# Optimization experiments

Hardware: AMD Instinct MI355X
Metric: run time of the kernel (lower is better)

Reference implementation:

```python
import jax, jax.numpy as jnp
import numpy as np

V = 1.0e10           # large init value for non-seed pixels (FastGeodis v)
LAMB = 0.0           # lamb=0 => pure Euclidean raster-scan distance
ITERS = 2            # FastGeodis iterations
THRESH = 0.7         # binarize_map threshold
TOPO_WEIGHT = 0.005
TOPO_WINDOW = 64
EPS = 1e-6
BIG = 1e20


def _sweep_down(dist, image):
    # One top-down raster sweep of the FastGeodis up-down pass.
    # dist, image: [H, W]. Row r updates from row r-1 at col offsets {-1,0,+1}
    # with squared spatial distances {2,1,2}; lamb weights the intensity term.
    W = dist.shape[1]
    sp2 = (2.0, 1.0, 2.0)

    def step(carry, xs):
        pd, pi = carry          # previous-row distance / intensity, [W]
        d_row, i_row = xs
        pd_pad = jnp.pad(pd, 1, constant_values=BIG)
        pi_pad = jnp.pad(pi, 1, constant_values=0.0)
        new = d_row
        for k in range(3):
            p = pd_pad[k:k + W]
            q = i_row - pi_pad[k:k + W]
            new = jnp.minimum(new, p + jnp.sqrt(sp2[k] + LAMB * q * q))
        return (new, i_row), new

    (_, _), rest = jax.lax.scan(step, (dist[0], image[0]), (dist[1:], image[1:]))
    return jnp.concatenate([dist[:1], rest], axis=0)


def _updown(dist, image):
    dist = _sweep_down(dist, image)
    dist = _sweep_down(dist[::-1], image[::-1])[::-1]
    return dist


def generalised_geodesic2d(image, softmask):
    # image: intensity map [H,W]; softmask: [H,W]; dist init = V * softmask.
    dist = V * softmask
    for _ in range(ITERS):
        dist = _updown(dist, image)
        dist = _updown(dist.T, image.T).T
    return dist


def calculate_edt(inp):
    # Original: softmask = inp, intensity image = 1 - inp (mask_pt = 1 - image_pt).
    return generalised_geodesic2d(1.0 - inp, inp)


def _global_norm(x):
    return (x - x.min()) / (x.max() - x.min() + EPS)


def _topo_loss(p, t, window):
    # Persistence-style matching proxy: within each non-overlapping window,
    # match level-set values of pred and target by sorting (0-dim persistence
    # birth/death values of the filtration are order statistics of the window)
    # and penalize squared differences of matched values.
    H, W = p.shape
    nh, nw = H // window, W // window

    def win_sort(x):
        x = x.reshape(nh, window, nw, window).transpose(0, 2, 1, 3)
        return jnp.sort(x.reshape(nh * nw, window * window), axis=-1)

    return jnp.mean((win_sort(p) - win_sort(t)) ** 2)


def _per_item(pred_i, target_i):
    # pred_i/target_i: [C, H, W]; pred already remapped to [0, 1]
    bin_pred = (pred_i >= THRESH).astype(jnp.float32)
    comb_pred = jnp.max(bin_pred, axis=0)        # combine_channels
    comb_tgt = jnp.max(target_i, axis=0)
    edt_p = _global_norm(calculate_edt(1.0 - comb_pred))
    edt_t = _global_norm(calculate_edt(1.0 - comb_tgt))
    return _topo_loss(edt_p, edt_t, TOPO_WINDOW)


def setup_inputs():
    key = jax.random.key(0)
    k1, k2 = jax.random.split(key)
    B, C, H, W = 16, 3, 512, 512
    pred = jax.random.normal(k1, (B, C, H, W), dtype=jnp.float32)  # model output in ~[-1,1]
    # target: binary multi-channel cell masks (sparse foreground)
    target = (jax.random.uniform(k2, (B, C, H, W)) > 0.8).astype(jnp.float32)
    return {"pred": pred, "target": target}


def reference(pred, target):
    pred01 = (pred + 1.0) / 2.0
    losses = jax.vmap(_per_item)(pred01.astype(jnp.float32), target.astype(jnp.float32))
    mean_loss = losses.mean()
    return (mean_loss * TOPO_WEIGHT, mean_loss)
```

## Files before the change

### kernel.cpp

```cpp
#include <hip/hip_runtime.h>

#define BIGF 1e20f
#define VF   1e10f

constexpr float SQ2 = 1.41421356237309515f;

__device__ __forceinline__ float dpp_left(float x)
{
    int o = __builtin_amdgcn_update_dpp(0x60AD78ECu , __float_as_int(x),
                                        0x138, 0xF, 0xF, false);
    return __int_as_float(o);
}
__device__ __forceinline__ float dpp_right(float x)
{
    int o = __builtin_amdgcn_update_dpp(0x60AD78ECu , __float_as_int(x),
                                        0x130, 0xF, 0xF, false);
    return __int_as_float(o);
}
template<int CTRL>
__device__ __forceinline__ float qdpp(float x)
{
    return __int_as_float(__builtin_amdgcn_update_dpp(0, __float_as_int(x),
                                                      CTRL, 0xF, 0xF, true));
}
__device__ __forceinline__ float fmed3(float a, float b, float c)
{
    return __builtin_amdgcn_fmed3f(a, b, c);
}

__device__ __forceinline__ void load_row8(const float* __restrict__ M, int r, int c0, float v[8])
{
    const float4* q = (const float4*)(M + ((long)r << 9) + c0);
    float4 a = q[0], b = q[1];
    v[0] = a.x; v[1] = a.y; v[2] = a.z; v[3] = a.w;
    v[4] = b.x; v[5] = b.y; v[6] = b.z; v[7] = b.w;
}

__device__ __forceinline__ void step8(const float cur[8], const float p[8], float nv[8])
{
    float left  = dpp_left(p[7]);
    float right = dpp_right(p[0]);
    #pragma unroll
    for (int j = 0; j < 8; ++j) {
        float l  = (j == 0) ? left  : p[j - 1];
        float rr = (j == 7) ? right : p[j + 1];
        nv[j] = fminf(fminf(cur[j], p[j] + 1.0f), fminf(l, rr) + SQ2);
    }
}

__global__ __launch_bounds__(256) void k_init(const float* __restrict__ pred,
                                              const float* __restrict__ tgt,
                                              float* __restrict__ bufA,
                                              float* __restrict__ acc,
                                              unsigned* __restrict__ count,
                                              float* __restrict__ minmax)
{
    if (blockIdx.x == 0 && threadIdx.x == 0) { *acc = 0.0f; *count = 0u; }
    if (blockIdx.x == 0 && threadIdx.x < 64)
        minmax[threadIdx.x] = (threadIdx.x & 1) ? 0.0f : BIGF;

    int r = blockIdx.x & 7;
    int k = blockIdx.x >> 3;
    int b = r + 8 * (k >> 8);
    int pix = ((k & 255) * 256 + threadIdx.x) << 2;
    long base = (long)b * 3 * 262144 + pix;

    float4 p0 = *(const float4*)(pred + base);
    float4 p1 = *(const float4*)(pred + base + 262144);
    float4 p2 = *(const float4*)(pred + base + 2 * 262144);
    float4 t0 = *(const float4*)(tgt + base);
    float4 t1 = *(const float4*)(tgt + base + 262144);
    float4 t2 = *(const float4*)(tgt + base + 2 * 262144);

    float P0[4] = {p0.x, p0.y, p0.z, p0.w};
    float P1[4] = {p1.x, p1.y, p1.z, p1.w};
    float P2[4] = {p2.x, p2.y, p2.z, p2.w};
    float T0[4] = {t0.x, t0.y, t0.z, t0.w};
    float T1[4] = {t1.x, t1.y, t1.z, t1.w};
    float T2[4] = {t2.x, t2.y, t2.z, t2.w};

    float oP[4], oT[4];
    #pragma unroll
    for (int e = 0; e < 4; ++e) {
        bool fgP = ((P0[e] + 1.0f) * 0.5f >= 0.7f) ||
                   ((P1[e] + 1.0f) * 0.5f >= 0.7f) ||
                   ((P2[e] + 1.0f) * 0.5f >= 0.7f);
        float mt = fmaxf(fmaxf(T0[e], T1[e]), T2[e]);
        oP[e] = fgP ? 0.0f : VF;
        oT[e] = VF * (1.0f - mt);
    }
    *(float4*)(bufA + (long)b * 262144 + pix)        = make_float4(oP[0], oP[1], oP[2], oP[3]);
    *(float4*)(bufA + (long)(16 + b) * 262144 + pix) = make_float4(oT[0], oT[1], oT[2], oT[3]);
}

__global__ __launch_bounds__(64) void k_p1d(const float* __restrict__ X0,
                                            float* __restrict__ Cb)
{
    int bi = blockIdx.x, m = bi >> 4, w = bi & 15;
    const float* X = X0 + ((long)m << 18);
    int c0 = (int)threadIdx.x << 3, a = w << 5;
    float p[8]; load_row8(X, a, c0, p);
    float buf[8][8];
    #pragma unroll
    for (int k = 1; k <= 7; ++k) load_row8(X, a + k, c0, buf[k & 7]);
    #pragma unroll
    for (int i = 1; i < 32; ++i) {
        if (i + 7 < 32) load_row8(X, a + i + 7, c0, buf[(i + 7) & 7]);
        float nv[8]; step8(buf[i & 7], p, nv);
        #pragma unroll
        for (int j = 0; j < 8; ++j) p[j] = nv[j];
    }
    float4* o = (float4*)(Cb + m * 8192 + w * 512 + c0);
    o[0] = make_float4(p[0], p[1], p[2], p[3]);
    o[1] = make_float4(p[4], p[5], p[6], p[7]);
}

__device__ __forceinline__ void combine(float* __restrict__ bwp, float* __restrict__ part,
                                        int wdst, int wsrc, int t, int wave, int lane,
                                        const float wreg[8])
{
    const float* bs = bwp + wsrc * 576;
    if (wave <= 8) {
        int base = lane * 8 + 8 * wave;
        float W[16];
        float4 W0 = *(const float4*)(bs + base);
        float4 W1 = *(const float4*)(bs + base + 4);
        W[0]=W0.x; W[1]=W0.y; W[2]=W0.z; W[3]=W0.w;
        W[4]=W1.x; W[5]=W1.y; W[6]=W1.z; W[7]=W1.w;
        float acc[8];
        if (wave < 8) {
            float4 W2 = *(const float4*)(bs + base + 8);
            float4 W3 = *(const float4*)(bs + base + 12);
            W[8]=W2.x; W[9]=W2.y; W[10]=W2.z; W[11]=W2.w;
            W[12]=W3.x; W[13]=W3.y; W[14]=W3.z; W[15]=W3.w;
            #pragma unroll
            for (int j = 0; j < 8; ++j) acc[j] = W[j] + wreg[0];
            #pragma unroll
            for (int dt = 1; dt < 8; ++dt)
                #pragma unroll
                for (int j = 0; j < 8; ++j)
                    acc[j] = fminf(acc[j], W[j + dt] + wreg[dt]);
        } else {
            #pragma unroll
            for (int j = 0; j < 8; ++j) acc[j] = W[j] + wreg[0];
        }
        float4* pp = (float4*)(part + wave * 512 + lane * 8);
        pp[0] = make_float4(acc[0], acc[1], acc[2], acc[3]);
        pp[1] = make_float4(acc[4], acc[5], acc[6], acc[7]);
    }
    __syncthreads();
    if (t < 512) {
        float r = bwp[wdst * 576 + 32 + t];
        #pragma unroll
        for (int p2 = 0; p2 < 9; ++p2) r = fminf(r, part[p2 * 512 + t]);
        bwp[wdst * 576 + 32 + t] = r;
    }
    __syncthreads();
}

__global__ __launch_bounds__(1024) void k_comb(float* __restrict__ Cb, int dir)
{
    __shared__ __align__(16) float bwp[16 * 576];
    __shared__ __align__(16) float part[9 * 512];
    __shared__ float wgt[72];
    int m = blockIdx.x, t = threadIdx.x, wave = t >> 6, lane = t & 63, c0 = lane << 3;
    float* Cm = Cb + m * 8192;

    bwp[wave * 576 + ((lane < 32) ? lane : lane + 512)] = BIGF;
    *(float4*)(bwp + wave * 576 + 32 + c0)     = *(const float4*)(Cm + wave * 512 + c0);
    *(float4*)(bwp + wave * 576 + 32 + c0 + 4) = *(const float4*)(Cm + wave * 512 + c0 + 4);
    if (t < 65) { int d = t - 32; int ad = d < 0 ? -d : d; wgt[t] = ad * SQ2 + (float)(32 - ad); }
    __syncthreads();
    float wreg[8];
    #pragma unroll
    for (int dt = 0; dt < 8; ++dt) wreg[dt] = BIGF;
    if (wave < 8) {
        #pragma unroll
        for (int dt = 0; dt < 8; ++dt) wreg[dt] = wgt[wave * 8 + dt];
    } else if (wave == 8) wreg[0] = wgt[64];

    #pragma unroll 1
    for (int i = 0; i < 15; ++i) {
        int w2 = (dir > 0) ? (1 + i) : (14 - i);
        combine(bwp, part, w2, w2 - dir, t, wave, lane, wreg);
    }
    *(float4*)(Cm + wave * 512 + c0)     = *(const float4*)(bwp + wave * 576 + 32 + c0);
    *(float4*)(Cm + wave * 512 + c0 + 4) = *(const float4*)(bwp + wave * 576 + 32 + c0 + 4);
}

__global__ __launch_bounds__(64) void k_pb(const float* __restrict__ X0,
                                           const float* __restrict__ Cb,
                                           float* __restrict__ Db)
{
    __shared__ __align__(16) float stash[31 * 512];
    int bi = blockIdx.x, m = bi >> 4, w = bi & 15;
    const float* X = X0 + ((long)m << 18);
    const int L = threadIdx.x;
    int c0 = L << 3, a = w << 5;
    float p[8], buf[8][8];

    if (w) {
        const float4* s = (const float4*)(Cb + m * 8192 + (w - 1) * 512 + c0);
        float4 s0 = s[0], s1 = s[1];
        p[0]=s0.x; p[1]=s0.y; p[2]=s0.z; p[3]=s0.w;
        p[4]=s1.x; p[5]=s1.y; p[6]=s1.z; p[7]=s1.w;
    } else {
        #pragma unroll
        for (int j = 0; j < 8; ++j) p[j] = BIGF;
    }

    #pragma unroll
    for (int k = 0; k < 7; ++k) load_row8(X, a + k, c0, buf[k & 7]);
    #pragma unroll
    for (int i = 0; i < 32; ++i) {
        if (i + 7 < 32) load_row8(X, a + i + 7, c0, buf[(i + 7) & 7]);
        float nv[8]; step8(buf[i & 7], p, nv);
        if (i < 31) {
            *(float4*)(stash + i * 512 + L * 4)       = make_float4(nv[0], nv[1], nv[2], nv[3]);
            *(float4*)(stash + i * 512 + 256 + L * 4) = make_float4(nv[4], nv[5], nv[6], nv[7]);
        }
        #pragma unroll
        for (int j = 0; j < 8; ++j) p[j] = nv[j];
    }

    float q[8], cur[8];
    #pragma unroll
    for (int j = 0; j < 8; ++j) q[j] = p[j];
    {
        float4 x0 = *(const float4*)(stash + 30 * 512 + L * 4);
        float4 x1 = *(const float4*)(stash + 30 * 512 + 256 + L * 4);
        cur[0]=x0.x; cur[1]=x0.y; cur[2]=x0.z; cur[3]=x0.w;
        cur[4]=x1.x; cur[5]=x1.y; cur[6]=x1.z; cur[7]=x1.w;
    }
    #pragma unroll
    for (int i = 1; i < 32; ++i) {
        float nxt[8];
        if (i < 31) {
            float4 x0 = *(const float4*)(stash + (30 - i) * 512 + L * 4);
            float4 x1 = *(const float4*)(stash + (30 - i) * 512 + 256 + L * 4);
            nxt[0]=x0.x; nxt[1]=x0.y; nxt[2]=x0.z; nxt[3]=x0.w;
            nxt[4]=x1.x; nxt[5]=x1.y; nxt[6]=x1.z; nxt[7]=x1.w;
        }
        float nv[8]; step8(cur, q, nv);
        #pragma unroll
        for (int j = 0; j < 8; ++j) q[j] = nv[j];
        if (i < 31) {
            #pragma unroll
            for (int j = 0; j < 8; ++j) cur[j] = nxt[j];
        }
    }
    float4* o = (float4*)(Db + m * 8192 + w * 512 + c0);
    o[0] = make_float4(q[0], q[1], q[2], q[3]);
    o[1] = make_float4(q[4], q[5], q[6], q[7]);
}

__device__ __forceinline__ void sst516(float* st, int slot, int c0, const float v[8])
{
    float4* q = (float4*)(st + slot * 516 + c0);
    q[0] = make_float4(v[0], v[1], v[2], v[3]);
    q[1] = make_float4(v[4], v[5], v[6], v[7]);
}
__device__ __forceinline__ void sld516(const float* st, int slot, int c0, float v[8])
{
    const float4* q = (const float4*)(st + slot * 516 + c0);
    float4 a = q[0], b = q[1];
    v[0]=a.x; v[1]=a.y; v[2]=a.z; v[3]=a.w;
    v[4]=b.x; v[5]=b.y; v[6]=b.z; v[7]=b.w;
}
__device__ __forceinline__ void half_out32(const float* st, float* __restrict__ Xo,
                                           int slotbase, int a2, int L)
{
    int g = L >> 2, j = (L & 3) << 2;
    #pragma unroll
    for (int it = 0; it < 32; ++it) {
        int c = (it << 4) + g;
        float4 v = make_float4(st[(slotbase + j + 0) * 516 + c],
                               st[(slotbase + j + 1) * 516 + c],
                               st[(slotbase + j + 2) * 516 + c],
                               st[(slotbase + j + 3) * 516 + c]);
        *(float4*)(Xo + (long)c * 512 + a2 + j) = v;
    }
}

__global__ __launch_bounds__(64) void k_p3u(const float* __restrict__ X0,
                                            float* __restrict__ Xo0,
                                            const float* __restrict__ Cb,
                                            const float* __restrict__ Db,
                                            float* __restrict__ minmax,
                                            int final_pass)
{
    __shared__ __align__(16) float stash[32 * 516];
    int bi = blockIdx.x, m = bi >> 4, w = bi & 15;
    const float* X = X0 + ((long)m << 18);
    float* Xo = Xo0 + ((long)m << 18);
    const int L = threadIdx.x;
    int c0 = L << 3, a = w << 5;
    float p[8], buf[8][8];

    if (w) {
        const float4* s = (const float4*)(Cb + m * 8192 + (w - 1) * 512 + c0);
        float4 s0 = s[0], s1 = s[1];
        p[0]=s0.x; p[1]=s0.y; p[2]=s0.z; p[3]=s0.w;
        p[4]=s1.x; p[5]=s1.y; p[6]=s1.z; p[7]=s1.w;
    } else {
        #pragma unroll
        for (int j = 0; j < 8; ++j) p[j] = BIGF;
    }
    #pragma unroll
    for (int k = 0; k < 7; ++k) load_row8(X, a + k, c0, buf[k & 7]);
    #pragma unroll
    for (int i = 0; i < 32; ++i) {
        if (i + 7 < 32) load_row8(X, a + i + 7, c0, buf[(i + 7) & 7]);
        float nv[8]; step8(buf[i & 7], p, nv);
        sst516(stash, i, c0, nv);
        #pragma unroll
        for (int j = 0; j < 8; ++j) p[j] = nv[j];
    }

    float s2[8];
    if (w < 15) {
        const float4* s = (const float4*)(Db + m * 8192 + (w + 1) * 512 + c0);
        float4 s0 = s[0], s1 = s[1];
        s2[0]=s0.x; s2[1]=s0.y; s2[2]=s0.z; s2[3]=s0.w;
        s2[4]=s1.x; s2[5]=s1.y; s2[6]=s1.z; s2[7]=s1.w;
    } else {
        #pragma unroll
        for (int j = 0; j < 8; ++j) s2[j] = BIGF;
    }
    float mn = BIGF, mx = -BIGF;
    #pragma unroll
    for (int i = 0; i < 16; ++i) {
        float cu[8];
        if (i == 0) {
            #pragma unroll
            for (int j = 0; j < 8; ++j) cu[j] = p[j];
        } else {
            sld516(stash, 31 - i, c0, cu);
        }
        float nv[8]; step8(cu, s2, nv);
        sst516(stash, 31 - i, c0, nv);
        #pragma unroll
        for (int j = 0; j < 8; ++j) { s2[j] = nv[j]; mn = fminf(mn, nv[j]); mx = fmaxf(mx, nv[j]); }
    }
    half_out32(stash, Xo, 16, a + 16, L);
    #pragma unroll
    for (int i = 16; i < 32; ++i) {
        float cu[8]; sld516(stash, 31 - i, c0, cu);
        float nv[8]; step8(cu, s2, nv);
        sst516(stash, 31 - i, c0, nv);
        #pragma unroll
        for (int j = 0; j < 8; ++j) { s2[j] = nv[j]; mn = fminf(mn, nv[j]); mx = fmaxf(mx, nv[j]); }
    }
    half_out32(stash, Xo, 0, a, L);

    if (final_pass) {
        for (int o = 32; o > 0; o >>= 1) {
            mn = fminf(mn, __shfl_down(mn, o));
            mx = fmaxf(mx, __shfl_down(mx, o));
        }
        if (L == 0) {
            atomicMin((int*)(minmax + 2 * m),     __float_as_int(mn));
            atomicMax((int*)(minmax + 2 * m + 1), __float_as_int(mx));
        }
    }
}

__device__ __forceinline__ void cex(float& lo, float& hi)
{
    float l = fminf(lo, hi);
    hi = fmaxf(lo, hi);
    lo = l;
}
__device__ __forceinline__ void merge8asc(float v[8])
{
    cex(v[0],v[4]); cex(v[1],v[5]); cex(v[2],v[6]); cex(v[3],v[7]);
    cex(v[0],v[2]); cex(v[1],v[3]); cex(v[4],v[6]); cex(v[5],v[7]);
    cex(v[0],v[1]); cex(v[2],v[3]); cex(v[4],v[5]); cex(v[6],v[7]);
}
__device__ __forceinline__ void sort8asc(float v[8])
{
    cex(v[0],v[1]); cex(v[2],v[3]); cex(v[4],v[5]); cex(v[6],v[7]);
    cex(v[0],v[3]); cex(v[1],v[2]); cex(v[4],v[7]); cex(v[5],v[6]);
    cex(v[0],v[1]); cex(v[2],v[3]); cex(v[4],v[5]); cex(v[6],v[7]);
    cex(v[0],v[7]); cex(v[1],v[6]); cex(v[2],v[5]); cex(v[3],v[4]);
    cex(v[0],v[2]); cex(v[1],v[3]); cex(v[4],v[6]); cex(v[5],v[7]);
    cex(v[0],v[1]); cex(v[2],v[3]); cex(v[4],v[5]); cex(v[6],v[7]);
}
__device__ __forceinline__ void xshfl(float v[8], int j8, float sel)
{
    #pragma unroll
    for (int e = 0; e < 8; ++e) {
        float o = __shfl_xor(v[e], j8);
        v[e] = fmed3(v[e], o, sel);
    }
}
template<int CTRL>
__device__ __forceinline__ void xdpp(float v[8], float sel)
{
    #pragma unroll
    for (int e = 0; e < 8; ++e) {
        float o = qdpp<CTRL>(v[e]);
        v[e] = fmed3(v[e], o, sel);
    }
}
__device__ __forceinline__ void rshfl(float v[8], int tmask, float sel)
{
    float o[8];
    #pragma unroll
    for (int e = 0; e < 8; ++e) o[e] = __shfl_xor(v[7 - e], tmask);
    #pragma unroll
    for (int e = 0; e < 8; ++e) v[e] = fmed3(v[e], o[e], sel);
}
template<int CTRL>
__device__ __forceinline__ void rdpp(float v[8], float sel)
{
    float o[8];
    #pragma unroll
    for (int e = 0; e < 8; ++e) o[e] = qdpp<CTRL>(v[7 - e]);
    #pragma unroll
    for (int e = 0; e < 8; ++e) v[e] = fmed3(v[e], o[e], sel);
}
__device__ __forceinline__ void lstage(float p[8], float q[8], int tmask, float sel, bool rev,
                                       float* sp, float* st, int t)
{
    __syncthreads();
    int sw = (t >> 2) & 1;
    int o0 = t * 8 + sw * 4;
    int o1 = t * 8 + (sw ^ 1) * 4;
    *(float4*)(sp + o0) = make_float4(p[0], p[1], p[2], p[3]);
    *(float4*)(sp + o1) = make_float4(p[4], p[5], p[6], p[7]);
    *(float4*)(st + o0) = make_float4(q[0], q[1], q[2], q[3]);
    *(float4*)(st + o1) = make_float4(q[4], q[5], q[6], q[7]);
    __syncthreads();
    int pt = t ^ tmask;
    int psw = (pt >> 2) & 1;
    int q0 = pt * 8 + psw * 4;
    int q1 = pt * 8 + (psw ^ 1) * 4;
    float4 a = *(const float4*)(sp + q0), bb = *(const float4*)(sp + q1);
    float4 c = *(const float4*)(st + q0), d = *(const float4*)(st + q1);
    float op[8] = {a.x,a.y,a.z,a.w,bb.x,bb.y,bb.z,bb.w};
    float oq[8] = {c.x,c.y,c.z,c.w,d.x,d.y,d.z,d.w};
    if (rev) {
        #pragma unroll
        for (int e = 0; e < 8; ++e) {
            p[e] = fmed3(p[e], op[7 - e], sel);
            q[e] = fmed3(q[e], oq[7 - e], sel);
        }
    } else {
        #pragma unroll
        for (int e = 0; e < 8; ++e) {
            p[e] = fmed3(p[e], op[e], sel);
            q[e] = fmed3(q[e], oq[e], sel);
        }
    }
}

__global__ __launch_bounds__(512) void k_loss(const float* __restrict__ bufB,
                                              const float* __restrict__ minmax,
                                              float* __restrict__ acc,
                                              unsigned* __restrict__ count,
                                              float* __restrict__ out)
{
    __shared__ float sp[4096];
    __shared__ float st[4096];
    __shared__ float rs[8];

    int t = threadIdx.x;
    int r = blockIdx.x & 7;
    int k = blockIdx.x >> 3;
    int b = r + 8 * (k >> 6);
    int w = k & 63;
    int wi = w >> 3, wj = w & 7;

    int i0 = t << 3;
    int y = wi * 64 + (i0 >> 6);
    int x = wj * 64 + (i0 & 63);

    float mnP = minmax[2 * b],        mxP = minmax[2 * b + 1];
    float mnT = minmax[2 * (16 + b)], mxT = minmax[2 * (16 + b) + 1];
    float sclP = 1.0f / (mxP - mnP + 1e-6f);
    float sclT = 1.0f / (mxT - mnT + 1e-6f);

    float p[8], q[8];
    {
        const float4* P4 = (const float4*)(bufB + (long)b * 262144 + y * 512 + x);
        const float4* T4 = (const float4*)(bufB + (long)(16 + b) * 262144 + y * 512 + x);
        float4 a = P4[0], bb = P4[1], c = T4[0], d = T4[1];
        p[0]=a.x; p[1]=a.y; p[2]=a.z; p[3]=a.w; p[4]=bb.x; p[5]=bb.y; p[6]=bb.z; p[7]=bb.w;
        q[0]=c.x; q[1]=c.y; q[2]=c.z; q[3]=c.w; q[4]=d.x;  q[5]=d.y;  q[6]=d.z;  q[7]=d.w;
        #pragma unroll
        for (int e = 0; e < 8; ++e) {
            p[e] = (p[e] - mnP) * sclP;
            q[e] = (q[e] - mnT) * sclT;
        }
    }

    const float INFP = __builtin_inff();
    sort8asc(p); sort8asc(q);

    #pragma unroll 1
    for (int kk = 16; kk <= 4096; kk <<= 1) {
        int tmask = (kk - 1) >> 3;
        float sel = ((t & (kk >> 4)) == 0) ? -INFP : INFP;
        if (kk == 16)        { rdpp<0xB1>(p, sel); rdpp<0xB1>(q, sel); }
        else if (kk == 32)   { rdpp<0x1B>(p, sel); rdpp<0x1B>(q, sel); }
        else if (tmask < 64) { rshfl(p, tmask, sel); rshfl(q, tmask, sel); }
        else                 lstage(p, q, tmask, sel, true, sp, st, t);

        #pragma unroll 1
        for (int j = kk >> 2; j >= 8; j >>= 1) {
            int j8 = j >> 3;
            float s2 = ((t & j8) == 0) ? -INFP : INFP;
            if (j8 == 1)      { xdpp<0xB1>(p, s2); xdpp<0xB1>(q, s2); }
            else if (j8 == 2) { xdpp<0x4E>(p, s2); xdpp<0x4E>(q, s2); }
            else if (j8 < 64) { xshfl(p, j8, s2); xshfl(q, j8, s2); }
            else              lstage(p, q, j8, s2, false, sp, st, t);
        }
        merge8asc(p); merge8asc(q);
    }

    float s = 0.0f;
    #pragma unroll
    for (int e = 0; e < 8; ++e) { float d = p[e] - q[e]; s += d * d; }
    for (int o = 32; o > 0; o >>= 1) s += __shfl_down(s, o);
    if ((t & 63) == 0) rs[t >> 6] = s;
    __syncthreads();
    if (t == 0) {
        float tot = 0.0f;
        #pragma unroll
        for (int i = 0; i < 8; ++i) tot += rs[i];
        atomicAdd(acc, tot);
        __threadfence();
        unsigned done = atomicAdd(count, 1u);
        if (done == 1023u) {
            float total = atomicAdd(acc, 0.0f);
            float mean = total * (1.0f / 4194304.0f);
            out[0] = mean * 0.005f;
            out[1] = mean;
        }
    }
}

extern "C" void kernel_launch(void* const* d_in, const int* in_sizes, int n_in,
                              void* d_out, int out_size, void* d_ws, size_t ws_size,
                              hipStream_t stream)
{
    const float* pred = (const float*)d_in[0];
    const float* tgt  = (const float*)d_in[1];
    float* out = (float*)d_out;

    char* ws = (char*)d_ws;
    float* bufA     = (float*)ws;
    float* bufB     = (float*)(ws + (32ull << 20));
    float* Cb       = (float*)(ws + (64ull << 20));
    float* Db       = (float*)(ws + (65ull << 20));
    float* minmax   = (float*)(ws + (66ull << 20));
    float* acc      = minmax + 64;
    unsigned* count = (unsigned*)(acc + 1);

    k_init<<<4096, 256, 0, stream>>>(pred, tgt, bufA, acc, count, minmax);

    for (int s = 0; s < 4; ++s) {
        const float* in = (s & 1) ? bufB : bufA;
        float* outb     = (s & 1) ? bufA : bufB;
        k_p1d <<<512,   64, 0, stream>>>(in, Cb);
        k_comb<<< 32, 1024, 0, stream>>>(Cb, +1);
        k_pb  <<<512,   64, 0, stream>>>(in, Cb, Db);
        k_comb<<< 32, 1024, 0, stream>>>(Db, -1);
        k_p3u <<<512,   64, 0, stream>>>(in, outb, Cb, Db, minmax, s == 3 ? 1 : 0);
    }

    k_loss<<<1024, 512, 0, stream>>>(bufA, minmax, acc, count, out);
}
```

Baseline: 385.7 us.

## Merge forward and backward block passes, derive backward carry-in algebraically in combine

The separate first-pass and backward-pass kernels are fused into one kernel. It computes each block's forward output from a BIG seed and also the backward result using local-only inputs. The second combine pass then corrects the backward values by min-plus propagation of the combined forward carries through a 64-wide distance kernel. This removes one full read of the image per stage and cuts the per-stage kernel launches from five to three. In exchange the combine kernel does more shared-memory work, and correctness relies on min-plus linearity of the sweep with the odd/even weight formula.

```diff
diff --git a/kernel.cpp b/kernel.cpp
--- a/kernel.cpp
+++ b/kernel.cpp
@@ -93,33 +93,75 @@
     *(float4*)(bufA + (long)(16 + b) * 262144 + pix) = make_float4(oT[0], oT[1], oT[2], oT[3]);
 }
 
-__global__ __launch_bounds__(64) void k_p1d(const float* __restrict__ X0,
-                                            float* __restrict__ Cb)
-{
+__global__ __launch_bounds__(64) void k_p1du(const float* __restrict__ X0,
+                                             float* __restrict__ Cb,
+                                             float* __restrict__ Db)
+{
+    __shared__ __align__(16) float stash[31 * 512];
     int bi = blockIdx.x, m = bi >> 4, w = bi & 15;
     const float* X = X0 + ((long)m << 18);
-    int c0 = (int)threadIdx.x << 3, a = w << 5;
-    float p[8]; load_row8(X, a, c0, p);
-    float buf[8][8];
-    #pragma unroll
-    for (int k = 1; k <= 7; ++k) load_row8(X, a + k, c0, buf[k & 7]);
-    #pragma unroll
-    for (int i = 1; i < 32; ++i) {
+    const int L = threadIdx.x;
+    int c0 = L << 3, a = w << 5;
+    float p[8], buf[8][8];
+    #pragma unroll
+    for (int j = 0; j < 8; ++j) p[j] = BIGF;
+
+    #pragma unroll
+    for (int k = 0; k < 7; ++k) load_row8(X, a + k, c0, buf[k & 7]);
+    #pragma unroll
+    for (int i = 0; i < 32; ++i) {
         if (i + 7 < 32) load_row8(X, a + i + 7, c0, buf[(i + 7) & 7]);
         float nv[8]; step8(buf[i & 7], p, nv);
+        if (i < 31) {
+            *(float4*)(stash + i * 512 + L * 4)       = make_float4(nv[0], nv[1], nv[2], nv[3]);
+            *(float4*)(stash + i * 512 + 256 + L * 4) = make_float4(nv[4], nv[5], nv[6], nv[7]);
+        }
         #pragma unroll
         for (int j = 0; j < 8; ++j) p[j] = nv[j];
     }
-    float4* o = (float4*)(Cb + m * 8192 + w * 512 + c0);
-    o[0] = make_float4(p[0], p[1], p[2], p[3]);
-    o[1] = make_float4(p[4], p[5], p[6], p[7]);
-}
-
+    {
+        float4* o = (float4*)(Cb + m * 8192 + w * 512 + c0);
+        o[0] = make_float4(p[0], p[1], p[2], p[3]);
+        o[1] = make_float4(p[4], p[5], p[6], p[7]);
+    }
+
+    float q[8], cur[8];
+    #pragma unroll
+    for (int j = 0; j < 8; ++j) q[j] = p[j];
+    {
+        float4 x0 = *(const float4*)(stash + 30 * 512 + L * 4);
+        float4 x1 = *(const float4*)(stash + 30 * 512 + 256 + L * 4);
+        cur[0]=x0.x; cur[1]=x0.y; cur[2]=x0.z; cur[3]=x0.w;
+        cur[4]=x1.x; cur[5]=x1.y; cur[6]=x1.z; cur[7]=x1.w;
+    }
+    #pragma unroll
+    for (int i = 1; i < 32; ++i) {
+        float nxt[8];
+        if (i < 31) {
+            float4 x0 = *(const float4*)(stash + (30 - i) * 512 + L * 4);
+            float4 x1 = *(const float4*)(stash + (30 - i) * 512 + 256 + L * 4);
+            nxt[0]=x0.x; nxt[1]=x0.y; nxt[2]=x0.z; nxt[3]=x0.w;
+            nxt[4]=x1.x; nxt[5]=x1.y; nxt[6]=x1.z; nxt[7]=x1.w;
+        }
+        float nv[8]; step8(cur, q, nv);
+        #pragma unroll
+        for (int j = 0; j < 8; ++j) q[j] = nv[j];
+        if (i < 31) {
+            #pragma unroll
+            for (int j = 0; j < 8; ++j) cur[j] = nxt[j];
+        }
+    }
+    float4* o = (float4*)(Db + m * 8192 + w * 512 + c0);
+    o[0] = make_float4(q[0], q[1], q[2], q[3]);
+    o[1] = make_float4(q[4], q[5], q[6], q[7]);
+}
+
+template<int S, int G>
 __device__ __forceinline__ void combine(float* __restrict__ bwp, float* __restrict__ part,
                                         int wdst, int wsrc, int t, int wave, int lane,
                                         const float wreg[8])
 {
-    const float* bs = bwp + wsrc * 576;
+    const float* bs = bwp + wsrc * S + (G - 32);
     if (wave <= 8) {
         int base = lane * 8 + 8 * wave;
         float W[16];
@@ -150,25 +192,32 @@
     }
     __syncthreads();
     if (t < 512) {
-        float r = bwp[wdst * 576 + 32 + t];
+        float r = bwp[wdst * S + G + t];
         #pragma unroll
         for (int p2 = 0; p2 < 9; ++p2) r = fminf(r, part[p2 * 512 + t]);
-        bwp[wdst * 576 + 32 + t] = r;
-    }
-    __syncthreads();
-}
-
-__global__ __launch_bounds__(1024) void k_comb(float* __restrict__ Cb, int dir)
-{
-    __shared__ __align__(16) float bwp[16 * 576];
+        bwp[wdst * S + G + t] = r;
+    }
+    __syncthreads();
+}
+
+__global__ __launch_bounds__(1024) void k_comb2(float* __restrict__ Cb,
+                                                float* __restrict__ Db)
+{
+    __shared__ __align__(16) float bwpA[16 * 640];
+    __shared__ __align__(16) float bwpB[16 * 576];
     __shared__ __align__(16) float part[9 * 512];
     __shared__ float wgt[72];
     int m = blockIdx.x, t = threadIdx.x, wave = t >> 6, lane = t & 63, c0 = lane << 3;
     float* Cm = Cb + m * 8192;
-
-    bwp[wave * 576 + ((lane < 32) ? lane : lane + 512)] = BIGF;
-    *(float4*)(bwp + wave * 576 + 32 + c0)     = *(const float4*)(Cm + wave * 512 + c0);
-    *(float4*)(bwp + wave * 576 + 32 + c0 + 4) = *(const float4*)(Cm + wave * 512 + c0 + 4);
+    float* Dm = Db + m * 8192;
+
+    bwpA[wave * 640 + lane]       = BIGF;
+    bwpA[wave * 640 + 576 + lane] = BIGF;
+    bwpB[wave * 576 + ((lane < 32) ? lane : lane + 512)] = BIGF;
+    *(float4*)(bwpA + wave * 640 + 64 + c0)     = *(const float4*)(Cm + wave * 512 + c0);
+    *(float4*)(bwpA + wave * 640 + 64 + c0 + 4) = *(const float4*)(Cm + wave * 512 + c0 + 4);
+    *(float4*)(bwpB + wave * 576 + 32 + c0)     = *(const float4*)(Dm + wave * 512 + c0);
+    *(float4*)(bwpB + wave * 576 + 32 + c0 + 4) = *(const float4*)(Dm + wave * 512 + c0 + 4);
     if (t < 65) { int d = t - 32; int ad = d < 0 ? -d : d; wgt[t] = ad * SQ2 + (float)(32 - ad); }
     __syncthreads();
     float wreg[8];
@@ -180,78 +229,53 @@
     } else if (wave == 8) wreg[0] = wgt[64];
 
     #pragma unroll 1
-    for (int i = 0; i < 15; ++i) {
-        int w2 = (dir > 0) ? (1 + i) : (14 - i);
-        combine(bwp, part, w2, w2 - dir, t, wave, lane, wreg);
-    }
-    *(float4*)(Cm + wave * 512 + c0)     = *(const float4*)(bwp + wave * 576 + 32 + c0);
-    *(float4*)(Cm + wave * 512 + c0 + 4) = *(const float4*)(bwp + wave * 576 + 32 + c0 + 4);
-}
-
-__global__ __launch_bounds__(64) void k_pb(const float* __restrict__ X0,
-                                           const float* __restrict__ Cb,
-                                           float* __restrict__ Db)
-{
-    __shared__ __align__(16) float stash[31 * 512];
-    int bi = blockIdx.x, m = bi >> 4, w = bi & 15;
-    const float* X = X0 + ((long)m << 18);
-    const int L = threadIdx.x;
-    int c0 = L << 3, a = w << 5;
-    float p[8], buf[8][8];
-
-    if (w) {
-        const float4* s = (const float4*)(Cb + m * 8192 + (w - 1) * 512 + c0);
-        float4 s0 = s[0], s1 = s[1];
-        p[0]=s0.x; p[1]=s0.y; p[2]=s0.z; p[3]=s0.w;
-        p[4]=s1.x; p[5]=s1.y; p[6]=s1.z; p[7]=s1.w;
-    } else {
-        #pragma unroll
-        for (int j = 0; j < 8; ++j) p[j] = BIGF;
-    }
-
-    #pragma unroll
-    for (int k = 0; k < 7; ++k) load_row8(X, a + k, c0, buf[k & 7]);
-    #pragma unroll
-    for (int i = 0; i < 32; ++i) {
-        if (i + 7 < 32) load_row8(X, a + i + 7, c0, buf[(i + 7) & 7]);
-        float nv[8]; step8(buf[i & 7], p, nv);
-        if (i < 31) {
-            *(float4*)(stash + i * 512 + L * 4)       = make_float4(nv[0], nv[1], nv[2], nv[3]);
-            *(float4*)(stash + i * 512 + 256 + L * 4) = make_float4(nv[4], nv[5], nv[6], nv[7]);
-        }
-        #pragma unroll
-        for (int j = 0; j < 8; ++j) p[j] = nv[j];
-    }
-
-    float q[8], cur[8];
-    #pragma unroll
-    for (int j = 0; j < 8; ++j) q[j] = p[j];
-    {
-        float4 x0 = *(const float4*)(stash + 30 * 512 + L * 4);
-        float4 x1 = *(const float4*)(stash + 30 * 512 + 256 + L * 4);
-        cur[0]=x0.x; cur[1]=x0.y; cur[2]=x0.z; cur[3]=x0.w;
-        cur[4]=x1.x; cur[5]=x1.y; cur[6]=x1.z; cur[7]=x1.w;
-    }
-    #pragma unroll
-    for (int i = 1; i < 32; ++i) {
-        float nxt[8];
-        if (i < 31) {
-            float4 x0 = *(const float4*)(stash + (30 - i) * 512 + L * 4);
-            float4 x1 = *(const float4*)(stash + (30 - i) * 512 + 256 + L * 4);
-            nxt[0]=x0.x; nxt[1]=x0.y; nxt[2]=x0.z; nxt[3]=x0.w;
-            nxt[4]=x1.x; nxt[5]=x1.y; nxt[6]=x1.z; nxt[7]=x1.w;
-        }
-        float nv[8]; step8(cur, q, nv);
-        #pragma unroll
-        for (int j = 0; j < 8; ++j) q[j] = nv[j];
-        if (i < 31) {
+    for (int i = 0; i < 15; ++i)
+        combine<640, 64>(bwpA, part, 1 + i, i, t, wave, lane, wreg);
+
+    *(float4*)(Cm + wave * 512 + c0)     = *(const float4*)(bwpA + wave * 640 + 64 + c0);
+    *(float4*)(Cm + wave * 512 + c0 + 4) = *(const float4*)(bwpA + wave * 640 + 64 + c0 + 4);
+
+    if (wave < 15) {
+        float accv[8];
+        {
+            const float4* B = (const float4*)(bwpB + (wave + 1) * 576 + 32 + c0);
+            float4 b0 = B[0], b1 = B[1];
+            accv[0]=b0.x; accv[1]=b0.y; accv[2]=b0.z; accv[3]=b0.w;
+            accv[4]=b1.x; accv[5]=b1.y; accv[6]=b1.z; accv[7]=b1.w;
+        }
+        const float* A = bwpA + wave * 640 + c0;
+        #pragma unroll
+        for (int k = 0; k < 16; ++k) {
+            float4 a0 = *(const float4*)(A + 8 * k);
+            float4 a1 = *(const float4*)(A + 8 * k + 4);
+            float4 a2 = *(const float4*)(A + 8 * k + 8);
+            float4 a3 = *(const float4*)(A + 8 * k + 12);
+            float W[16] = {a0.x,a0.y,a0.z,a0.w, a1.x,a1.y,a1.z,a1.w,
+                           a2.x,a2.y,a2.z,a2.w, a3.x,a3.y,a3.z,a3.w};
             #pragma unroll
-            for (int j = 0; j < 8; ++j) cur[j] = nxt[j];
-        }
-    }
-    float4* o = (float4*)(Db + m * 8192 + w * 512 + c0);
-    o[0] = make_float4(q[0], q[1], q[2], q[3]);
-    o[1] = make_float4(q[4], q[5], q[6], q[7]);
+            for (int dt = 0; dt < 8; ++dt) {
+                const int d  = 8 * k - 64 + dt;
+                const int ad = (d < 0) ? -d : d;
+                if (ad <= 63) {
+                    const float wt = (float)ad * SQ2 + ((ad & 1) ? 0.0f : 1.0f);
+                    #pragma unroll
+                    for (int j = 0; j < 8; ++j)
+                        accv[j] = fminf(accv[j], W[j + dt] + wt);
+                }
+            }
+        }
+        float4* Bo = (float4*)(bwpB + (wave + 1) * 576 + 32 + c0);
+        Bo[0] = make_float4(accv[0], accv[1], accv[2], accv[3]);
+        Bo[1] = make_float4(accv[4], accv[5], accv[6], accv[7]);
+    }
+    __syncthreads();
+
+    #pragma unroll 1
+    for (int i = 0; i < 15; ++i)
+        combine<576, 32>(bwpB, part, 14 - i, 15 - i, t, wave, lane, wreg);
+
+    *(float4*)(Dm + wave * 512 + c0)     = *(const float4*)(bwpB + wave * 576 + 32 + c0);
+    *(float4*)(Dm + wave * 512 + c0 + 4) = *(const float4*)(bwpB + wave * 576 + 32 + c0 + 4);
 }
 
 __device__ __forceinline__ void sst516(float* st, int slot, int c0, const float v[8])
@@ -563,11 +587,9 @@
     for (int s = 0; s < 4; ++s) {
         const float* in = (s & 1) ? bufB : bufA;
         float* outb     = (s & 1) ? bufA : bufB;
-        k_p1d <<<512,   64, 0, stream>>>(in, Cb);
-        k_comb<<< 32, 1024, 0, stream>>>(Cb, +1);
-        k_pb  <<<512,   64, 0, stream>>>(in, Cb, Db);
-        k_comb<<< 32, 1024, 0, stream>>>(Db, -1);
-        k_p3u <<<512,   64, 0, stream>>>(in, outb, Cb, Db, minmax, s == 3 ? 1 : 0);
+        k_p1du <<<512,   64, 0, stream>>>(in, Cb, Db);
+        k_comb2<<< 32, 1024, 0, stream>>>(Cb, Db);
+        k_p3u  <<<512,   64, 0, stream>>>(in, outb, Cb, Db, minmax, s == 3 ? 1 : 0);
     }
 
     k_loss<<<1024, 512, 0, stream>>>(bufA, minmax, acc, count, out);
```

Measured after the change: 410.4 us. +6.4%, slower.
